# Kernel tuning notes

Measured on AMD Instinct MI355X. Metric: run time of the kernel, lower is better.

## Reference

```python
import jax, jax.numpy as jnp
import numpy as np

N_NODES = 100000
N_EDGES = 1600000
NFEAT = 256
NHID = 128


def setup_inputs() -> dict:
    key = jax.random.key(0)
    k1, k2, k3, k4, k5 = jax.random.split(key, 5)
    x = jax.random.normal(k1, (N_NODES, NFEAT), dtype=jnp.float32)
    edge_src = jax.random.randint(k2, (N_EDGES,), 0, N_NODES, dtype=jnp.int64)
    edge_dst = jax.random.randint(k3, (N_EDGES,), 0, N_NODES, dtype=jnp.int64)
    edge_w = jax.random.uniform(k4, (N_EDGES,), dtype=jnp.float32)
    W = jax.random.normal(k5, (NFEAT, NHID), dtype=jnp.float32) * (1.0 / np.sqrt(NFEAT))
    b = jnp.zeros((NHID,), dtype=jnp.float32)
    return {"x": x, "edge_src": edge_src, "edge_dst": edge_dst, "edge_w": edge_w, "W": W, "b": b}


def reference(x, edge_src, edge_dst, edge_w, W, b):
    # GraphConvolution: support = x @ W ; out = spmm(adj, support) + b ; then ReLU
    support = x @ W                                  # [N, nhid]
    msgs = support[edge_src] * edge_w[:, None]       # [E, nhid] gather + scale
    agg = jax.ops.segment_sum(msgs, edge_dst, num_segments=N_NODES)  # [N, nhid]
    return jax.nn.relu(agg + b)
```

## Files before the change

### kernel.cpp

```cpp
#include <hip/hip_runtime.h>
#include <hip/hip_bf16.h>

#define NFEAT 256
#define NHID  128
#define NPB   128
#define BMAX  2048
#define SCHUNK 2048

typedef short s16x8 __attribute__((ext_vector_type(8)));
typedef float f32x4 __attribute__((ext_vector_type(4)));
typedef float f32x2 __attribute__((ext_vector_type(2)));

static __device__ __forceinline__ ushort bfbits(float f) {
  __hip_bfloat16 h = __float2bfloat16(f);
  return *reinterpret_cast<ushort*>(&h);
}

__device__ __forceinline__ void gemm_tile(
    const float* __restrict__ x, const ushort* __restrict__ Wt,
    ushort* __restrict__ sup, int n_nodes, int rowBase,
    ushort* As, ushort* Bs) {
  const int t = threadIdx.x;
  const int wid = t >> 6;
  const int lane = t & 63;
  if (rowBase >= n_nodes) return;

  f32x4 acc[4][2];
#pragma unroll
  for (int m = 0; m < 4; ++m)
#pragma unroll
    for (int n = 0; n < 2; ++n) acc[m][n] = (f32x4){0.f, 0.f, 0.f, 0.f};

  const float4* x4 = (const float4*)x;

  for (int kc = 0; kc < 4; ++kc) {
    __syncthreads();
#pragma unroll
    for (int it = 0; it < 4; ++it) {
      const int i4 = t + it * 256;
      const int r = i4 >> 4, k4 = i4 & 15;
      const int row = rowBase + r;
      float4 v = make_float4(0.f, 0.f, 0.f, 0.f);
      if (row < n_nodes) v = x4[(size_t)row * (NFEAT / 4) + kc * 16 + k4];
      ushort4 h;
      h.x = bfbits(v.x); h.y = bfbits(v.y); h.z = bfbits(v.z); h.w = bfbits(v.w);
      int byte = (r << 7) + (k4 << 3);
      byte ^= (r & 7) << 4;
      *(ushort4*)((char*)As + byte) = h;
    }
#pragma unroll
    for (int it = 0; it < 8; ++it) {
      const int i2 = t + it * 256;
      const int col = i2 >> 4, k4 = i2 & 15;
      const ushort4 h = *(const ushort4*)(Wt + col * NFEAT + kc * 64 + k4 * 4);
      int byte = (col << 7) + (k4 << 3);
      byte ^= (col & 7) << 4;
      *(ushort4*)((char*)Bs + byte) = h;
    }
    __syncthreads();
#pragma unroll
    for (int ks = 0; ks < 2; ++ks) {
      const int k0 = ks * 32 + (lane >> 4) * 8;
      s16x8 af[4], bfr[2];
#pragma unroll
      for (int m = 0; m < 4; ++m) {
        const int r = m * 16 + (lane & 15);
        int byte = (r << 7) + (k0 << 1);
        byte ^= (r & 7) << 4;
        af[m] = *(const s16x8*)((const char*)As + byte);
      }
#pragma unroll
      for (int n = 0; n < 2; ++n) {
        const int c = wid * 32 + n * 16 + (lane & 15);
        int byte = (c << 7) + (k0 << 1);
        byte ^= (c & 7) << 4;
        bfr[n] = *(const s16x8*)((const char*)Bs + byte);
      }
#pragma unroll
      for (int m = 0; m < 4; ++m)
#pragma unroll
        for (int n = 0; n < 2; ++n)
          acc[m][n] = __builtin_amdgcn_mfma_f32_16x16x32_bf16(af[m], bfr[n], acc[m][n], 0, 0, 0);
    }
  }

#pragma unroll
  for (int m = 0; m < 4; ++m) {
#pragma unroll
    for (int rr = 0; rr < 4; ++rr) {
      const int row = rowBase + m * 16 + (lane >> 4) * 4 + rr;
      if (row < n_nodes) {
#pragma unroll
        for (int n = 0; n < 2; ++n) {
          const int col = wid * 32 + n * 16 + (lane & 15);
          sup[(size_t)row * NHID + col] = bfbits(acc[m][n][rr]);
        }
      }
    }
  }
}

__global__ __launch_bounds__(256) void prep_kernel(
    const float* __restrict__ W, ushort* __restrict__ Wt,
    const int* __restrict__ edst, int* __restrict__ histT,
    int n_edges, int B, int G) {
  __shared__ int hist[BMAX];
  if (blockIdx.x < 128) {
    const int id = blockIdx.x * 256 + threadIdx.x;
    const int k = id >> 7, n = id & 127;
    Wt[n * NFEAT + k] = bfbits(W[id]);
    return;
  }
  const int g = blockIdx.x - 128;
  for (int b = threadIdx.x; b < B; b += 256) hist[b] = 0;
  __syncthreads();
  const int e0 = g * SCHUNK;
  const int e1 = (e0 + SCHUNK < n_edges) ? e0 + SCHUNK : n_edges;
  for (int e = e0 + threadIdx.x; e < e1; e += 256)
    atomicAdd(&hist[(uint)edst[e] >> 7], 1);
  __syncthreads();
  for (int b = threadIdx.x; b < B; b += 256) histT[(size_t)b * G + g] = hist[b];
}

__global__ __launch_bounds__(256) void scan1_kernel(
    const int* __restrict__ in, int* __restrict__ exc,
    int* __restrict__ bsums, int n) {
  const int tid = threadIdx.x;
  const int lane = tid & 63, wid = tid >> 6;
  const int base = blockIdx.x * 1024 + tid * 4;
  int v0 = 0, v1 = 0, v2 = 0, v3 = 0;
  if (base + 3 < n) {
    int4 v = *(const int4*)(in + base);
    v0 = v.x; v1 = v.y; v2 = v.z; v3 = v.w;
  } else {
    if (base + 0 < n) v0 = in[base + 0];
    if (base + 1 < n) v1 = in[base + 1];
    if (base + 2 < n) v2 = in[base + 2];
  }
  const int tsum = v0 + v1 + v2 + v3;
  int t = tsum;
#pragma unroll
  for (int d = 1; d < 64; d <<= 1) {
    int u = __shfl_up(t, d);
    if (lane >= d) t += u;
  }
  __shared__ int wtot[4], wpre[4];
  if (lane == 63) wtot[wid] = t;
  __syncthreads();
  if (tid == 0) {
    int s = 0;
    for (int w = 0; w < 4; ++w) { wpre[w] = s; s += wtot[w]; }
    bsums[blockIdx.x] = s;
  }
  __syncthreads();
  const int off = (t - tsum) + wpre[wid];
  if (base + 0 < n) exc[base + 0] = off;
  if (base + 1 < n) exc[base + 1] = off + v0;
  if (base + 2 < n) exc[base + 2] = off + v0 + v1;
  if (base + 3 < n) exc[base + 3] = off + v0 + v1 + v2;
}

__global__ __launch_bounds__(256) void scan2_kernel(int* __restrict__ bsums, int nb) {
  __shared__ int wtot[4], wpre[4], tot_s;
  const int tid = threadIdx.x;
  const int lane = tid & 63, wid = tid >> 6;
  int carry = 0;
  for (int base = 0; base < nb; base += 256) {
    const int idx = base + tid;
    const int v = (idx < nb) ? bsums[idx] : 0;
    int t = v;
#pragma unroll
    for (int d = 1; d < 64; d <<= 1) {
      int u = __shfl_up(t, d);
      if (lane >= d) t += u;
    }
    if (lane == 63) wtot[wid] = t;
    __syncthreads();
    if (tid == 0) {
      int s = 0;
      for (int w = 0; w < 4; ++w) { wpre[w] = s; s += wtot[w]; }
      tot_s = s;
    }
    __syncthreads();
    if (idx < nb) bsums[idx] = carry + (t - v) + wpre[wid];
    carry += tot_s;
    __syncthreads();
  }
}

__global__ __launch_bounds__(256) void scan3_kernel(
    const int* __restrict__ exc, const int* __restrict__ bsums,
    int* __restrict__ baseT, int* __restrict__ bucket_start,
    int n, int G, int B, int n_edges) {
  const int i = blockIdx.x * 256 + threadIdx.x;
  if (i < n) {
    const int v = exc[i] + bsums[i >> 10];
    const int b = i / G, g = i % G;
    baseT[(size_t)g * B + b] = v;
    if (g == 0) bucket_start[b] = v;
  }
  if (i == 0) bucket_start[B] = n_edges;
}

__global__ __launch_bounds__(256) void fusedA_kernel(
    const float* __restrict__ x, const ushort* __restrict__ Wt,
    ushort* __restrict__ sup, int n_nodes,
    const int* __restrict__ esrc, const int* __restrict__ edst,
    const float* __restrict__ ew, const int* __restrict__ baseT,
    int2* __restrict__ packed2, int n_edges, int B, int G, int nA) {
  __shared__ ushort As[64 * 64];
  __shared__ ushort Bs[128 * 64];

  const int idx = blockIdx.x;
  const long long total = (long long)nA + G;
  const int c_lo = (int)((long long)idx * G / total);
  const int c_hi = (int)(((long long)idx + 1) * G / total);
  int role, sub;
  if (c_hi > c_lo) { role = 0; sub = c_lo; }
  else             { role = 1; sub = idx - c_hi; }

  if (role == 0) {
    int* cursor = (int*)As;
    const int g = sub;
    for (int b = threadIdx.x; b < B; b += 256) cursor[b] = baseT[(size_t)g * B + b];
    __syncthreads();
    const int e0 = g * SCHUNK;
    if (e0 + SCHUNK <= n_edges) {
      int d[8], s[8]; float w[8];
#pragma unroll
      for (int j = 0; j < 8; ++j) {
        const int e = e0 + j * 256 + threadIdx.x;
        d[j] = edst[e]; s[j] = esrc[e]; w[j] = ew[e];
      }
#pragma unroll
      for (int j = 0; j < 8; ++j) {
        const int pos = atomicAdd(&cursor[(uint)d[j] >> 7], 1);
        packed2[pos] = make_int2(s[j] | ((d[j] & (NPB - 1)) << 18), __float_as_int(w[j]));
      }
    } else {
      for (int e = e0 + threadIdx.x; e < n_edges; e += 256) {
        const int dst = edst[e];
        const int pos = atomicAdd(&cursor[(uint)dst >> 7], 1);
        packed2[pos] = make_int2(esrc[e] | ((dst & (NPB - 1)) << 18), __float_as_int(ew[e]));
      }
    }
    return;
  }

  gemm_tile(x, Wt, sup, n_nodes, sub * 64, As, Bs);
}

__global__ __launch_bounds__(256) void fusedB_kernel(
    const float* __restrict__ x, const ushort* __restrict__ Wt,
    ushort* __restrict__ sup, int n_nodes,
    const int2* __restrict__ packed2, const int* __restrict__ bucket_start,
    int2* __restrict__ packedN, int* __restrict__ row_start,
    int n_edges, int B, int nB, int gemm_base) {
  __shared__ ushort As[64 * 64];
  __shared__ ushort Bs[128 * 64];
  __shared__ int cnt[NPB];
  __shared__ int st[NPB];
  __shared__ int cur[NPB];
  __shared__ int w0tot;

  const int idx = blockIdx.x;
  const long long total = (long long)nB + B;
  const int c_lo = (int)((long long)idx * B / total);
  const int c_hi = (int)(((long long)idx + 1) * B / total);
  int role, sub;
  if (c_hi > c_lo) { role = 0; sub = c_lo; }
  else             { role = 1; sub = idx - c_hi; }

  if (role == 0) {
    const int tid = threadIdx.x;
    const int b = sub;
    const int s0 = bucket_start[b];
    const int s1 = bucket_start[b + 1];
    const int m = s1 - s0;

    if (tid < NPB) cnt[tid] = 0;
    __syncthreads();

    for (int i = tid; i < m; i += 256)
      atomicAdd(&cnt[((uint)packed2[s0 + i].x >> 18) & (NPB - 1)], 1);
    __syncthreads();

    {
      const int v = (tid < NPB) ? cnt[tid] : 0;
      int t = v;
#pragma unroll
      for (int d = 1; d < 64; d <<= 1) {
        int u = __shfl_up(t, d);
        if ((tid & 63) >= d) t += u;
      }
      if (tid == 63) w0tot = t;
      __syncthreads();
      if (tid < NPB) {
        const int s = (t - v) + ((tid >= 64) ? w0tot : 0);
        st[tid] = s;
        cur[tid] = s;
      }
      __syncthreads();
    }

    for (int i = tid; i < m; i += 256) {
      const int2 e = packed2[s0 + i];
      const int dl = ((uint)e.x >> 18) & (NPB - 1);
      const int pos = atomicAdd(&cur[dl], 1);
      packedN[s0 + pos] = e;
    }

    if (tid < NPB) {
      const int node = b * NPB + tid;
      if (node < n_nodes) row_start[node] = s0 + st[tid];
    }
    if (b == 0 && tid == 0) row_start[n_nodes] = n_edges;
    return;
  }

  gemm_tile(x, Wt, sup, n_nodes, (gemm_base + sub) * 64, As, Bs);
}

__global__ __launch_bounds__(256) void agg_kernel(
    const ushort* __restrict__ sup, const int2* __restrict__ packed,
    const int* __restrict__ row_start, const float* __restrict__ bias,
    float* __restrict__ out, int n_nodes) {
  const int node = blockIdx.x * 4 + (threadIdx.x >> 6);
  if (node >= n_nodes) return;
  const int lane = threadIdx.x & 63;
  const int start = __builtin_amdgcn_readfirstlane(row_start[node]);
  const int end   = __builtin_amdgcn_readfirstlane(row_start[node + 1]);

  float a0 = 0.f, a1 = 0.f, b0 = 0.f, b1 = 0.f;
  float c0 = 0.f, c1 = 0.f, d0 = 0.f, d1 = 0.f;
  int i = start;
  for (; i + 7 < end; i += 8) {
    const int2 e0 = packed[i + 0];
    const int2 e1 = packed[i + 1];
    const int2 e2 = packed[i + 2];
    const int2 e3 = packed[i + 3];
    const int2 e4 = packed[i + 4];
    const int2 e5 = packed[i + 5];
    const int2 e6 = packed[i + 6];
    const int2 e7 = packed[i + 7];
    const uint u0 = *(const uint*)(sup + ((size_t)((uint)e0.x & 0x3FFFFu) << 7) + lane * 2);
    const uint u1 = *(const uint*)(sup + ((size_t)((uint)e1.x & 0x3FFFFu) << 7) + lane * 2);
    const uint u2 = *(const uint*)(sup + ((size_t)((uint)e2.x & 0x3FFFFu) << 7) + lane * 2);
    const uint u3 = *(const uint*)(sup + ((size_t)((uint)e3.x & 0x3FFFFu) << 7) + lane * 2);
    const uint u4 = *(const uint*)(sup + ((size_t)((uint)e4.x & 0x3FFFFu) << 7) + lane * 2);
    const uint u5 = *(const uint*)(sup + ((size_t)((uint)e5.x & 0x3FFFFu) << 7) + lane * 2);
    const uint u6 = *(const uint*)(sup + ((size_t)((uint)e6.x & 0x3FFFFu) << 7) + lane * 2);
    const uint u7 = *(const uint*)(sup + ((size_t)((uint)e7.x & 0x3FFFFu) << 7) + lane * 2);
    const float w0 = __int_as_float(e0.y), w1 = __int_as_float(e1.y);
    const float w2 = __int_as_float(e2.y), w3 = __int_as_float(e3.y);
    const float w4 = __int_as_float(e4.y), w5 = __int_as_float(e5.y);
    const float w6 = __int_as_float(e6.y), w7 = __int_as_float(e7.y);
    a0 += __uint_as_float(u0 << 16) * w0 + __uint_as_float(u4 << 16) * w4;
    a1 += __uint_as_float(u0 & 0xffff0000u) * w0 + __uint_as_float(u4 & 0xffff0000u) * w4;
    b0 += __uint_as_float(u1 << 16) * w1 + __uint_as_float(u5 << 16) * w5;
    b1 += __uint_as_float(u1 & 0xffff0000u) * w1 + __uint_as_float(u5 & 0xffff0000u) * w5;
    c0 += __uint_as_float(u2 << 16) * w2 + __uint_as_float(u6 << 16) * w6;
    c1 += __uint_as_float(u2 & 0xffff0000u) * w2 + __uint_as_float(u6 & 0xffff0000u) * w6;
    d0 += __uint_as_float(u3 << 16) * w3 + __uint_as_float(u7 << 16) * w7;
    d1 += __uint_as_float(u3 & 0xffff0000u) * w3 + __uint_as_float(u7 & 0xffff0000u) * w7;
  }
  for (; i + 3 < end; i += 4) {
    const int2 e0 = packed[i + 0];
    const int2 e1 = packed[i + 1];
    const int2 e2 = packed[i + 2];
    const int2 e3 = packed[i + 3];
    const uint u0 = *(const uint*)(sup + ((size_t)((uint)e0.x & 0x3FFFFu) << 7) + lane * 2);
    const uint u1 = *(const uint*)(sup + ((size_t)((uint)e1.x & 0x3FFFFu) << 7) + lane * 2);
    const uint u2 = *(const uint*)(sup + ((size_t)((uint)e2.x & 0x3FFFFu) << 7) + lane * 2);
    const uint u3 = *(const uint*)(sup + ((size_t)((uint)e3.x & 0x3FFFFu) << 7) + lane * 2);
    const float w0 = __int_as_float(e0.y), w1 = __int_as_float(e1.y);
    const float w2 = __int_as_float(e2.y), w3 = __int_as_float(e3.y);
    a0 += __uint_as_float(u0 << 16) * w0 + __uint_as_float(u2 << 16) * w2;
    a1 += __uint_as_float(u0 & 0xffff0000u) * w0 + __uint_as_float(u2 & 0xffff0000u) * w2;
    b0 += __uint_as_float(u1 << 16) * w1 + __uint_as_float(u3 << 16) * w3;
    b1 += __uint_as_float(u1 & 0xffff0000u) * w1 + __uint_as_float(u3 & 0xffff0000u) * w3;
  }
  for (; i < end; ++i) {
    const int2 e0 = packed[i];
    const uint u0 = *(const uint*)(sup + ((size_t)((uint)e0.x & 0x3FFFFu) << 7) + lane * 2);
    const float w0 = __int_as_float(e0.y);
    a0 += __uint_as_float(u0 << 16) * w0;
    a1 += __uint_as_float(u0 & 0xffff0000u) * w0;
  }

  const float2 bb = ((const float2*)bias)[lane];
  f32x2 r;
  r.x = fmaxf((a0 + b0) + (c0 + d0) + bb.x, 0.f);
  r.y = fmaxf((a1 + b1) + (c1 + d1) + bb.y, 0.f);
  __builtin_nontemporal_store(r, (f32x2*)out + (size_t)node * (NHID / 2) + lane);
}

__global__ __launch_bounds__(256) void scatter_bf16_kernel(
    const ushort* __restrict__ sup, const int* __restrict__ esrc,
    const int* __restrict__ edst, const float* __restrict__ ew,
    float* __restrict__ out, int n_edges) {
  const long long idx = (long long)blockIdx.x * 256 + threadIdx.x;
  const int e = (int)(idx >> 6);
  const int c2 = (int)(idx & 63);
  if (e >= n_edges) return;
  const int s = esrc[e];
  const int d = edst[e];
  const float wt = ew[e];
  const uint u = *(const uint*)(sup + (size_t)s * NHID + c2 * 2);
  float* drow = out + (size_t)d * NHID + c2 * 2;
  atomicAdd(drow + 0, __uint_as_float(u << 16) * wt);
  atomicAdd(drow + 1, __uint_as_float(u & 0xffff0000u) * wt);
}

__global__ __launch_bounds__(256) void bias_relu_kernel(
    float* __restrict__ out, const float* __restrict__ b, int n4) {
  const int i = blockIdx.x * 256 + threadIdx.x;
  if (i >= n4) return;
  float4 v = ((float4*)out)[i];
  const float4 bb = ((const float4*)b)[i & (NHID / 4 - 1)];
  v.x = fmaxf(v.x + bb.x, 0.f);
  v.y = fmaxf(v.y + bb.y, 0.f);
  v.z = fmaxf(v.z + bb.z, 0.f);
  v.w = fmaxf(v.w + bb.w, 0.f);
  ((float4*)out)[i] = v;
}

static inline size_t align_up(size_t v, size_t a) { return (v + a - 1) & ~(a - 1); }

extern "C" void kernel_launch(void* const* d_in, const int* in_sizes, int n_in,
                              void* d_out, int out_size, void* d_ws, size_t ws_size,
                              hipStream_t stream) {
  const float* x    = (const float*)d_in[0];
  const int*   esrc = (const int*)d_in[1];
  const int*   edst = (const int*)d_in[2];
  const float* ew   = (const float*)d_in[3];
  const float* W    = (const float*)d_in[4];
  const float* b    = (const float*)d_in[5];
  float* out = (float*)d_out;

  const int n_nodes = in_sizes[0] / NFEAT;
  const int n_edges = in_sizes[1];

  const int B = (n_nodes + NPB - 1) / NPB;
  const int G = (n_edges + SCHUNK - 1) / SCHUNK;
  const long long n_scan_ll = (long long)B * G;

  char* ws = (char*)d_ws;
  size_t off = 0;
  ushort* sup       = (ushort*)(ws + off); off = align_up(off + (size_t)n_nodes * NHID * 2, 256);
  ushort* Wt        = (ushort*)(ws + off); off = align_up(off + (size_t)NFEAT * NHID * 2, 256);
  int* histT        = (int*)(ws + off);    off = align_up(off + (size_t)B * G * 4, 256);
  int* exc          = (int*)(ws + off);    off = align_up(off + (size_t)B * G * 4, 256);
  int* baseT        = (int*)(ws + off);    off = align_up(off + (size_t)B * G * 4, 256);
  int* bsums        = (int*)(ws + off);    off = align_up(off + 1024 * 4, 256);
  int* bucket_start = (int*)(ws + off);    off = align_up(off + ((size_t)B + 1) * 4, 256);
  int* row_start    = (int*)(ws + off);    off = align_up(off + ((size_t)n_nodes + 1) * 4, 256);
  int2* packed2     = (int2*)(ws + off);   off = align_up(off + (size_t)n_edges * 8, 256);
  int2* packedN     = (int2*)(ws + off);   off = align_up(off + (size_t)n_edges * 8, 256);
  const bool csr_ok = (off <= ws_size) && (n_nodes <= 256 * 1024) && (B <= BMAX) &&
                      (n_scan_ll <= 1024 * 1024);

  const int n_gemm = (n_nodes + 63) / 64;
  const int nA = (n_gemm + 1) / 2;
  const int nB = n_gemm - nA;

  if (csr_ok) {
    prep_kernel<<<128 + G, 256, 0, stream>>>(W, Wt, edst, histT, n_edges, B, G);

    const int n_scan = (int)n_scan_ll;
    const int nb = (n_scan + 1023) / 1024;
    scan1_kernel<<<nb, 256, 0, stream>>>(histT, exc, bsums, n_scan);
    scan2_kernel<<<1, 256, 0, stream>>>(bsums, nb);
    scan3_kernel<<<(n_scan + 255) / 256, 256, 0, stream>>>(exc, bsums, baseT, bucket_start, n_scan, G, B, n_edges);

    fusedA_kernel<<<nA + G, 256, 0, stream>>>(
        x, Wt, sup, n_nodes, esrc, edst, ew, baseT, packed2, n_edges, B, G, nA);

    fusedB_kernel<<<nB + B, 256, 0, stream>>>(
        x, Wt, sup, n_nodes, packed2, bucket_start, packedN, row_start,
        n_edges, B, nB, nA);

    agg_kernel<<<(n_nodes + 3) / 4, 256, 0, stream>>>(sup, packedN, row_start, b, out, n_nodes);
  } else {
    prep_kernel<<<128, 256, 0, stream>>>(W, Wt, edst, (int*)d_ws, 0, 1, 1);
    fusedA_kernel<<<n_gemm, 256, 0, stream>>>(
        x, Wt, sup, n_nodes, esrc, edst, ew, (int*)d_ws, (int2*)d_ws,
        0, 1, 0, n_gemm);
    hipMemsetAsync(out, 0, (size_t)n_nodes * NHID * sizeof(float), stream);
    const long long threads = (long long)n_edges * 64;
    scatter_bf16_kernel<<<(int)((threads + 255) / 256), 256, 0, stream>>>(sup, esrc, edst, ew, out, n_edges);
    const int n4 = n_nodes * NHID / 4;
    bias_relu_kernel<<<(n4 + 255) / 256, 256, 0, stream>>>(out, b, n4);
  }
}
```

Baseline: 142.7 us.

## Split weight conversion out and spread GEMM tiles across three fused CSR stages

Splits the W-to-bf16 transpose into its own small kernel. The histogram stage becomes a fused kernel that also runs a fifth of the GEMM tiles, and the remaining tiles are split between the scatter stage and the per-bucket sort stage. The aim is to hide the memory-bound histogram pass behind GEMM work and balance each launch, at the cost of one extra kernel launch and a weight-conversion dependency ahead of the first fused stage.

Result: slower. 152.4 us (+6.8%).

```diff
diff --git a/kernel.cpp b/kernel.cpp
--- a/kernel.cpp
+++ b/kernel.cpp
@@ -14,6 +14,15 @@
 static __device__ __forceinline__ ushort bfbits(float f) {
   __hip_bfloat16 h = __float2bfloat16(f);
   return *reinterpret_cast<ushort*>(&h);
+}
+
+static __device__ __forceinline__ void role_map(int idx, int count0, int count1,
+                                                int& role, int& sub) {
+  const long long total = (long long)count0 + count1;
+  const int c_lo = (int)((long long)idx * count0 / total);
+  const int c_hi = (int)(((long long)idx + 1) * count0 / total);
+  if (c_hi > c_lo) { role = 0; sub = c_lo; }
+  else             { role = 1; sub = idx - c_hi; }
 }
 
 __device__ __forceinline__ void gemm_tile(
@@ -100,26 +109,39 @@
   }
 }
 
-__global__ __launch_bounds__(256) void prep_kernel(
-    const float* __restrict__ W, ushort* __restrict__ Wt,
+__global__ __launch_bounds__(256) void wcvt_kernel(
+    const float* __restrict__ W, ushort* __restrict__ Wt) {
+  const int id = blockIdx.x * 256 + threadIdx.x;
+  const int k = id >> 7, n = id & 127;
+  Wt[n * NFEAT + k] = bfbits(W[id]);
+}
+
+__global__ __launch_bounds__(256) void fused1_kernel(
+    const float* __restrict__ x, const ushort* __restrict__ Wt,
+    ushort* __restrict__ sup, int n_nodes,
     const int* __restrict__ edst, int* __restrict__ histT,
-    int n_edges, int B, int G) {
-  __shared__ int hist[BMAX];
-  if (blockIdx.x < 128) {
-    const int id = blockIdx.x * 256 + threadIdx.x;
-    const int k = id >> 7, n = id & 127;
-    Wt[n * NFEAT + k] = bfbits(W[id]);
+    int n_edges, int B, int G, int n1) {
+  __shared__ ushort As[64 * 64];
+  __shared__ ushort Bs[128 * 64];
+
+  int role, sub;
+  role_map(blockIdx.x, G, n1, role, sub);
+
+  if (role == 0) {
+    int* hist = (int*)As;
+    const int g = sub;
+    for (int b = threadIdx.x; b < B; b += 256) hist[b] = 0;
+    __syncthreads();
+    const int e0 = g * SCHUNK;
+    const int e1 = (e0 + SCHUNK < n_edges) ? e0 + SCHUNK : n_edges;
+    for (int e = e0 + threadIdx.x; e < e1; e += 256)
+      atomicAdd(&hist[(uint)edst[e] >> 7], 1);
+    __syncthreads();
+    for (int b = threadIdx.x; b < B; b += 256) histT[(size_t)b * G + g] = hist[b];
     return;
   }
-  const int g = blockIdx.x - 128;
-  for (int b = threadIdx.x; b < B; b += 256) hist[b] = 0;
-  __syncthreads();
-  const int e0 = g * SCHUNK;
-  const int e1 = (e0 + SCHUNK < n_edges) ? e0 + SCHUNK : n_edges;
-  for (int e = e0 + threadIdx.x; e < e1; e += 256)
-    atomicAdd(&hist[(uint)edst[e] >> 7], 1);
-  __syncthreads();
-  for (int b = threadIdx.x; b < B; b += 256) histT[(size_t)b * G + g] = hist[b];
+
+  gemm_tile(x, Wt, sup, n_nodes, sub * 64, As, Bs);
 }
 
 __global__ __launch_bounds__(256) void scan1_kernel(
@@ -202,22 +224,17 @@
   if (i == 0) bucket_start[B] = n_edges;
 }
 
-__global__ __launch_bounds__(256) void fusedA_kernel(
+__global__ __launch_bounds__(256) void fused2_kernel(
     const float* __restrict__ x, const ushort* __restrict__ Wt,
     ushort* __restrict__ sup, int n_nodes,
     const int* __restrict__ esrc, const int* __restrict__ edst,
     const float* __restrict__ ew, const int* __restrict__ baseT,
-    int2* __restrict__ packed2, int n_edges, int B, int G, int nA) {
+    int2* __restrict__ packed2, int n_edges, int B, int G, int n2, int gemm_base) {
   __shared__ ushort As[64 * 64];
   __shared__ ushort Bs[128 * 64];
 
-  const int idx = blockIdx.x;
-  const long long total = (long long)nA + G;
-  const int c_lo = (int)((long long)idx * G / total);
-  const int c_hi = (int)(((long long)idx + 1) * G / total);
   int role, sub;
-  if (c_hi > c_lo) { role = 0; sub = c_lo; }
-  else             { role = 1; sub = idx - c_hi; }
+  role_map(blockIdx.x, G, n2, role, sub);
 
   if (role == 0) {
     int* cursor = (int*)As;
@@ -247,15 +264,15 @@
     return;
   }
 
-  gemm_tile(x, Wt, sup, n_nodes, sub * 64, As, Bs);
-}
-
-__global__ __launch_bounds__(256) void fusedB_kernel(
+  gemm_tile(x, Wt, sup, n_nodes, (gemm_base + sub) * 64, As, Bs);
+}
+
+__global__ __launch_bounds__(256) void fused3_kernel(
     const float* __restrict__ x, const ushort* __restrict__ Wt,
     ushort* __restrict__ sup, int n_nodes,
     const int2* __restrict__ packed2, const int* __restrict__ bucket_start,
     int2* __restrict__ packedN, int* __restrict__ row_start,
-    int n_edges, int B, int nB, int gemm_base) {
+    int n_edges, int B, int n3, int gemm_base) {
   __shared__ ushort As[64 * 64];
   __shared__ ushort Bs[128 * 64];
   __shared__ int cnt[NPB];
@@ -263,13 +280,8 @@
   __shared__ int cur[NPB];
   __shared__ int w0tot;
 
-  const int idx = blockIdx.x;
-  const long long total = (long long)nB + B;
-  const int c_lo = (int)((long long)idx * B / total);
-  const int c_hi = (int)(((long long)idx + 1) * B / total);
   int role, sub;
-  if (c_hi > c_lo) { role = 0; sub = c_lo; }
-  else             { role = 1; sub = idx - c_hi; }
+  role_map(blockIdx.x, B, n3, role, sub);
 
   if (role == 0) {
     const int tid = threadIdx.x;
@@ -412,6 +424,14 @@
   atomicAdd(drow + 1, __uint_as_float(u & 0xffff0000u) * wt);
 }
 
+__global__ __launch_bounds__(256) void gemm_only_kernel(
+    const float* __restrict__ x, const ushort* __restrict__ Wt,
+    ushort* __restrict__ sup, int n_nodes) {
+  __shared__ ushort As[64 * 64];
+  __shared__ ushort Bs[128 * 64];
+  gemm_tile(x, Wt, sup, n_nodes, blockIdx.x * 64, As, Bs);
+}
+
 __global__ __launch_bounds__(256) void bias_relu_kernel(
     float* __restrict__ out, const float* __restrict__ b, int n4) {
   const int i = blockIdx.x * 256 + threadIdx.x;
@@ -461,11 +481,15 @@
                       (n_scan_ll <= 1024 * 1024);
 
   const int n_gemm = (n_nodes + 63) / 64;
-  const int nA = (n_gemm + 1) / 2;
-  const int nB = n_gemm - nA;
+  const int n1 = n_gemm / 5;
+  const int n2 = n_gemm / 2;
+  const int n3 = n_gemm - n1 - n2;
 
   if (csr_ok) {
-    prep_kernel<<<128 + G, 256, 0, stream>>>(W, Wt, edst, histT, n_edges, B, G);
+    wcvt_kernel<<<(NFEAT * NHID) / 256, 256, 0, stream>>>(W, Wt);
+
+    fused1_kernel<<<G + n1, 256, 0, stream>>>(
+        x, Wt, sup, n_nodes, edst, histT, n_edges, B, G, n1);
 
     const int n_scan = (int)n_scan_ll;
     const int nb = (n_scan + 1023) / 1024;
@@ -473,19 +497,17 @@
     scan2_kernel<<<1, 256, 0, stream>>>(bsums, nb);
     scan3_kernel<<<(n_scan + 255) / 256, 256, 0, stream>>>(exc, bsums, baseT, bucket_start, n_scan, G, B, n_edges);
 
-    fusedA_kernel<<<nA + G, 256, 0, stream>>>(
-        x, Wt, sup, n_nodes, esrc, edst, ew, baseT, packed2, n_edges, B, G, nA);
-
-    fusedB_kernel<<<nB + B, 256, 0, stream>>>(
+    fused2_kernel<<<G + n2, 256, 0, stream>>>(
+        x, Wt, sup, n_nodes, esrc, edst, ew, baseT, packed2, n_edges, B, G, n2, n1);
+
+    fused3_kernel<<<B + n3, 256, 0, stream>>>(
         x, Wt, sup, n_nodes, packed2, bucket_start, packedN, row_start,
-        n_edges, B, nB, nA);
+        n_edges, B, n3, n1 + n2);
 
     agg_kernel<<<(n_nodes + 3) / 4, 256, 0, stream>>>(sup, packedN, row_start, b, out, n_nodes);
   } else {
-    prep_kernel<<<128, 256, 0, stream>>>(W, Wt, edst, (int*)d_ws, 0, 1, 1);
-    fusedA_kernel<<<n_gemm, 256, 0, stream>>>(
-        x, Wt, sup, n_nodes, esrc, edst, ew, (int*)d_ws, (int2*)d_ws,
-        0, 1, 0, n_gemm);
+    wcvt_kernel<<<(NFEAT * NHID) / 256, 256, 0, stream>>>(W, Wt);
+    gemm_only_kernel<<<n_gemm, 256, 0, stream>>>(x, Wt, sup, n_nodes);
     hipMemsetAsync(out, 0, (size_t)n_nodes * NHID * sizeof(float), stream);
     const long long threads = (long long)n_edges * 64;
     scatter_bf16_kernel<<<(int)((threads + 255) / 256), 256, 0, stream>>>(sup, esrc, edst, ew, out, n_edges);
```
